# Kernel tuning notes

Hardware: AMD Instinct MI355X
Metric: run time of the kernel (lower is better)

The kernel has to match this reference:

```python
import jax, jax.numpy as jnp
import numpy as np

B, N, M, D, H, DFF = 1, 2048, 2048, 1024, 16, 4096
MASK_VAL = -50000.0
EPS = 1e-5


def _xavier(k, shape):
    lim = np.sqrt(6.0 / (shape[0] + shape[1])).astype(np.float32)
    return jax.random.uniform(k, shape, jnp.float32, -lim, lim)


def setup_inputs() -> dict:
    key = jax.random.key(0)
    ks = jax.random.split(key, 8)
    return {
        "x": jax.random.normal(ks[0], (B, N, D), jnp.float32),
        "context": jax.random.normal(ks[1], (B, M, D), jnp.float32),
        "Wq": _xavier(ks[2], (D, D)), "bq": jnp.zeros((D,), jnp.float32),
        "Wkv": _xavier(ks[3], (D, 2 * D)), "bkv": jnp.zeros((2 * D,), jnp.float32),
        "Wo": _xavier(ks[4], (D, D)), "bo": jnp.zeros((D,), jnp.float32),
        "ln1_g": jnp.ones((D,), jnp.float32), "ln1_b": jnp.zeros((D,), jnp.float32),
        "W1": _xavier(ks[5], (D, DFF)), "bf1": jnp.zeros((DFF,), jnp.float32),
        "W2": _xavier(ks[6], (DFF, D)), "bf2": jnp.zeros((D,), jnp.float32),
        "ln2_g": jnp.ones((D,), jnp.float32), "ln2_b": jnp.zeros((D,), jnp.float32),
    }


def _layernorm(x, g, b):
    mu = x.mean(-1, keepdims=True)
    var = ((x - mu) ** 2).mean(-1, keepdims=True)
    return (x - mu) * jax.lax.rsqrt(var + EPS) * g + b


def reference(x, context, Wq, bq, Wkv, bkv, Wo, bo, ln1_g, ln1_b, W1, bf1, W2, bf2, ln2_g, ln2_b):
    b, n, d = x.shape
    m = context.shape[1]
    h = H
    dh = d // h
    scale = dh ** -0.5
    # q from x only; k,v from [x; context]
    q = (x @ Wq + bq).reshape(b, n, h, dh).transpose(0, 2, 1, 3)          # b h n dh
    kv_in = jnp.concatenate([x, context], axis=1)                          # b (n+m) d
    k, v = jnp.split(kv_in @ Wkv + bkv, 2, axis=-1)
    k = k.reshape(b, n + m, h, dh).transpose(0, 2, 1, 3)                   # b h (n+m) dh
    v = v.reshape(b, n + m, h, dh).transpose(0, 2, 1, 3)
    dots = jnp.einsum('bhid,bhjd->bhij', q * scale, k)                     # b h n (n+m)
    # causal mask applies only to the self-attention (first n) key columns
    rows = jnp.arange(n)[:, None]
    cols = jnp.arange(n + m)[None, :]
    causal = (cols < n) & (cols > rows)
    dots = jnp.where(causal, MASK_VAL, dots)
    attn = jax.nn.softmax(dots, axis=-1)                                   # dropout = identity (eval)
    out = jnp.einsum('bhij,bhjd->bhid', attn, v)
    out = out.transpose(0, 2, 1, 3).reshape(b, n, d) @ Wo + bo
    # PostNorm(Residual(attn))
    x1 = _layernorm(x + out, ln1_g, ln1_b)
    # PostNorm(Residual(FFN)) with exact-erf GELU
    ff = jax.nn.gelu(x1 @ W1 + bf1, approximate=False) @ W2 + bf2
    return _layernorm(x1 + ff, ln2_g, ln2_b)
```

## Files before the change

### kernel.cpp

```cpp
#include <hip/hip_runtime.h>


using bf16x8 = __attribute__((ext_vector_type(8))) short;
using f32x4  = __attribute__((ext_vector_type(4))) float;

__device__ __forceinline__ ushort f2bf(float f) {
    unsigned u = __float_as_uint(f);
    unsigned r = (u + 0x7fffu + ((u >> 16) & 1u)) >> 16;
    return (ushort)r;
}

__device__ __forceinline__ void gload16(const void* g, void* l) {
    __builtin_amdgcn_global_load_lds(
        (const __attribute__((address_space(1))) void*)g,
        (__attribute__((address_space(3))) void*)l, 16, 0, 0);
}

__device__ __forceinline__ float gelu_erf(float v) {
    return 0.5f * v * (1.0f + erff(v * 0.70710678118654752f));
}

__device__ __forceinline__ uint cvtpk(float a, float b) {
    uint r;
    asm("v_cvt_pk_bf16_f32 %0, %1, %2" : "=v"(r) : "v"(a), "v"(b));
    return r;
}

__global__ __launch_bounds__(256) void cvt4(const float* __restrict__ in,
                                            ushort* __restrict__ out, int n) {
    int i = (blockIdx.x * 256 + threadIdx.x) * 4;
    if (i + 3 < n) {
        float4 v = *(const float4*)(in + i);
        ushort4 o;
        o.x = f2bf(v.x); o.y = f2bf(v.y); o.z = f2bf(v.z); o.w = f2bf(v.w);
        *(ushort4*)(out + i) = o;
    }
}

__global__ __launch_bounds__(256) void tcvt(const float* __restrict__ in,
                                            ushort* __restrict__ out, int R, int C) {
    __shared__ float tile[32][33];
    const int tx = threadIdx.x, ty = threadIdx.y;
    const int c0 = blockIdx.x * 32, r0 = blockIdx.y * 32;
#pragma unroll
    for (int i = 0; i < 4; ++i)
        tile[ty + 8 * i][tx] = in[(size_t)(r0 + ty + 8 * i) * C + c0 + tx];
    __syncthreads();
#pragma unroll
    for (int i = 0; i < 4; ++i)
        out[(size_t)(c0 + ty + 8 * i) * R + r0 + tx] = f2bf(tile[tx][ty + 8 * i]);
}

__global__ __launch_bounds__(256) void vtrans(const ushort* __restrict__ KV,
                                              ushort* __restrict__ Vt) {
    __shared__ ushort tile[32][34];
    const int tx = threadIdx.x, ty = threadIdx.y;
    const int j0 = blockIdx.x * 32, d0 = blockIdx.y * 32;
#pragma unroll
    for (int i = 0; i < 4; ++i)
        tile[ty + 8 * i][tx] = KV[(size_t)(j0 + ty + 8 * i) * 2048 + 1024 + d0 + tx];
    __syncthreads();
#pragma unroll
    for (int i = 0; i < 4; ++i)
        Vt[(size_t)(d0 + ty + 8 * i) * 4096 + j0 + tx] = tile[tx][ty + 8 * i];
}

template <int BM, int BN, int ACT, int OUTF32, int RES, int SCALED, int SPLITK>
__global__ __launch_bounds__(256) void gemm_bt(
    const ushort* __restrict__ A, int lda, const ushort* __restrict__ Bt, int ldb,
    const float* __restrict__ bias, const float* __restrict__ resid,
    void* __restrict__ Cout, int M, int N, int K, float scale) {
    constexpr int MR = BM / 32, NR = BN / 32;
    __shared__ __align__(16) ushort Asm[BM * 64];
    __shared__ __align__(16) ushort Bsm[BN * 64];
    const int tid = threadIdx.x;
    const int w = tid >> 6, lane = tid & 63, g = lane >> 4, i15 = lane & 15;
    const int wm = w >> 1, wn = w & 1;
    const int m0 = blockIdx.y * BM, n0 = blockIdx.x * BN;
    if (SPLITK) {
        A += (size_t)blockIdx.z * K;
        Bt += (size_t)blockIdx.z * K;
    }

    f32x4 acc[MR][NR] = {};

    for (int kt = 0; kt < K; kt += 64) {
#pragma unroll
        for (int q = 0; q < BM / 32; ++q) {
            int off = (w * (BM / 32) + q) * 1024 + lane * 16;
            int r = off >> 7, cb = off & 127;
            int scb = cb ^ ((r & 7) << 4);
            const void* src = (const char*)A + ((size_t)(m0 + r) * lda + kt) * 2 + scb;
            gload16(src, (char*)Asm + (w * (BM / 32) + q) * 1024);
        }
#pragma unroll
        for (int q = 0; q < BN / 32; ++q) {
            int off = (w * (BN / 32) + q) * 1024 + lane * 16;
            int r = off >> 7, cb = off & 127;
            int scb = cb ^ ((r & 7) << 4);
            const void* src = (const char*)Bt + ((size_t)(n0 + r) * ldb + kt) * 2 + scb;
            gload16(src, (char*)Bsm + (w * (BN / 32) + q) * 1024);
        }
        __syncthreads();

#pragma unroll
        for (int kc = 0; kc < 2; ++kc) {
            bf16x8 af[MR], bfr[NR];
#pragma unroll
            for (int mi = 0; mi < MR; ++mi) {
                int r = wm * (BM / 2) + mi * 16 + i15;
                af[mi] = *(const bf16x8*)((const char*)Asm + r * 128 +
                                          ((kc * 64 + g * 16) ^ ((r & 7) << 4)));
            }
#pragma unroll
            for (int ni = 0; ni < NR; ++ni) {
                int r = wn * (BN / 2) + ni * 16 + i15;
                bfr[ni] = *(const bf16x8*)((const char*)Bsm + r * 128 +
                                           ((kc * 64 + g * 16) ^ ((r & 7) << 4)));
            }
#pragma unroll
            for (int mi = 0; mi < MR; ++mi)
#pragma unroll
                for (int ni = 0; ni < NR; ++ni)
                    acc[mi][ni] = __builtin_amdgcn_mfma_f32_16x16x32_bf16(
                        af[mi], bfr[ni], acc[mi][ni], 0, 0, 0);
        }
        __syncthreads();
    }

    float* Cf = (float*)Cout;
    if (SPLITK) Cf += (size_t)blockIdx.z * M * N;

#pragma unroll
    for (int ni = 0; ni < NR; ++ni) {
        int col = n0 + wn * (BN / 2) + ni * 16 + i15;
        float bb = bias ? bias[col] : 0.f;
#pragma unroll
        for (int mi = 0; mi < MR; ++mi) {
#pragma unroll
            for (int r2 = 0; r2 < 4; ++r2) {
                int row = m0 + wm * (BM / 2) + mi * 16 + 4 * g + r2;
                float v = acc[mi][ni][r2] + bb;
                if (ACT) v = gelu_erf(v);
                if (SCALED) v *= scale;
                size_t off = (size_t)row * N + col;
                if (OUTF32) {
                    float rv = RES ? resid[off] : 0.f;
                    Cf[off] = v + rv;
                } else {
                    ((ushort*)Cout)[off] = f2bf(v);
                }
            }
        }
    }
}

template <int SPLIT>
__global__ __launch_bounds__(256) void flash_attn(
    const ushort* __restrict__ Q,
    const ushort* __restrict__ KVb,
    const ushort* __restrict__ Vt,
    ushort* __restrict__ O,
    float* __restrict__ Opart,
    float* __restrict__ Ml) {
    constexpr int D = 1024;
    __shared__ __align__(16) ushort Ksm[2][64 * 64];
    __shared__ __align__(16) ushort Vsm[2][64 * 64];
    __shared__ __align__(16) ushort Psm[4][16 * 64];

    const int tid = threadIdx.x;
    const int w = tid >> 6, lane = tid & 63, g = lane >> 4, i15 = lane & 15;
    const int bid = blockIdx.x;
    const int h = bid & 15;
    int qi, s;
    if (SPLIT) { qi = 31 - ((bid >> 4) >> 1); s = (bid >> 4) & 1; }
    else       { qi = 31 - (bid >> 4); s = 0; }
    const int qb = qi * 64;
    const int qrow = qb + w * 16 + i15;

    bf16x8 qf[2];
    qf[0] = *(const bf16x8*)(Q + (size_t)qrow * D + h * 64 + g * 8);
    qf[1] = *(const bf16x8*)(Q + (size_t)qrow * D + h * 64 + 32 + g * 8);

    f32x4 o[4] = {};
    float m_run = -INFINITY, l_run = 0.f;

    const int diag = qi;
    const int nt = diag + 33;
    const int lo = (SPLIT && s) ? (nt >> 1) : 0;
    const int hi = SPLIT ? (s ? nt : (nt >> 1)) : nt;

    const int sr  = tid >> 3;
    const int scb = (tid & 7) * 16;
    const int ssw = scb ^ ((sr & 7) << 4);
    const char* kb0 = (const char*)KVb + ((size_t)sr * 2048 + h * 64) * 2 + scb;
    const char* vb0 = (const char*)Vt + ((size_t)(h * 64 + sr) * 4096) * 2 + scb;

    uint4 kreg0, kreg1, vreg0, vreg1;
    auto jt_of = [&](int t) { return (t <= diag) ? t : (32 + (t - diag - 1)); };
    auto stage = [&](int jt) {
        const char* kb = kb0 + (size_t)jt * 64 * 2048 * 2;
        kreg0 = *(const uint4*)kb;
        kreg1 = *(const uint4*)(kb + 32 * 2048 * 2);
        const char* vb = vb0 + (size_t)jt * 64 * 2;
        vreg0 = *(const uint4*)vb;
        vreg1 = *(const uint4*)(vb + 32 * 4096 * 2);
    };
    auto wlds = [&](int buf) {
        *(uint4*)((char*)Ksm[buf] + sr * 128 + ssw) = kreg0;
        *(uint4*)((char*)Ksm[buf] + (sr + 32) * 128 + ssw) = kreg1;
        *(uint4*)((char*)Vsm[buf] + sr * 128 + ssw) = vreg0;
        *(uint4*)((char*)Vsm[buf] + (sr + 32) * 128 + ssw) = vreg1;
    };

    stage(jt_of(lo));
    wlds(0);
    __syncthreads();
    int cur = 0;

    const int pbase = i15 * 128;
    const int psw = (i15 & 7) << 4;

    for (int t = lo; t < hi; ++t) {
        const int jt = jt_of(t);
        const bool more = (t + 1 < hi);
        if (more) stage(jt_of(t + 1));

        f32x4 st[4];
#pragma unroll
        for (int jg = 0; jg < 4; ++jg) {
            int jr = jg * 16 + i15;
            bf16x8 ka0 = *(const bf16x8*)((const char*)Ksm[cur] + jr * 128 +
                                          ((g * 16) ^ ((jr & 7) << 4)));
            bf16x8 ka1 = *(const bf16x8*)((const char*)Ksm[cur] + jr * 128 +
                                          ((64 + g * 16) ^ ((jr & 7) << 4)));
            f32x4 z = {};
            z = __builtin_amdgcn_mfma_f32_16x16x32_bf16(ka0, qf[0], z, 0, 0, 0);
            z = __builtin_amdgcn_mfma_f32_16x16x32_bf16(ka1, qf[1], z, 0, 0, 0);
            st[jg] = z;
        }
        if (jt == diag) {
#pragma unroll
            for (int jg = 0; jg < 4; ++jg)
#pragma unroll
                for (int r = 0; r < 4; ++r) {
                    int j = jt * 64 + jg * 16 + 4 * g + r;
                    if (j > qrow) st[jg][r] = -50000.f;
                }
        }

        float v8[8];
#pragma unroll
        for (int jg = 0; jg < 4; ++jg) {
            v8[2 * jg]     = fmaxf(st[jg][0], st[jg][1]);
            v8[2 * jg + 1] = fmaxf(st[jg][2], st[jg][3]);
        }
        v8[0] = fmaxf(v8[0], v8[4]); v8[1] = fmaxf(v8[1], v8[5]);
        v8[2] = fmaxf(v8[2], v8[6]); v8[3] = fmaxf(v8[3], v8[7]);
        float mt = fmaxf(fmaxf(v8[0], v8[1]), fmaxf(v8[2], v8[3]));
        mt = fmaxf(mt, __shfl_xor(mt, 16));
        mt = fmaxf(mt, __shfl_xor(mt, 32));

        const bool skip = __all(mt - m_run <= 8.f);
        float mnew, fscale;
        if (skip) { mnew = m_run; fscale = 1.f; }
        else      { mnew = fmaxf(m_run, mt); fscale = exp2f(m_run - mnew); }

        float pf[4][4], sj[4];
#pragma unroll
        for (int jg = 0; jg < 4; ++jg) {
#pragma unroll
            for (int r = 0; r < 4; ++r) pf[jg][r] = exp2f(st[jg][r] - mnew);
            sj[jg] = (pf[jg][0] + pf[jg][1]) + (pf[jg][2] + pf[jg][3]);
        }
        float psum = (sj[0] + sj[1]) + (sj[2] + sj[3]);
        psum += __shfl_xor(psum, 16);
        psum += __shfl_xor(psum, 32);
        l_run = l_run * fscale + psum;
        m_run = mnew;

        if (!skip) {
#pragma unroll
            for (int r = 0; r < 4; ++r) {
                float fr = __shfl(fscale, 20 * g + r);
#pragma unroll
                for (int dg = 0; dg < 4; ++dg) o[dg][r] *= fr;
            }
        }

#pragma unroll
        for (int jg = 0; jg < 4; ++jg) {
            uint2 pk;
            pk.x = cvtpk(pf[jg][0], pf[jg][1]);
            pk.y = cvtpk(pf[jg][2], pf[jg][3]);
            *(uint2*)((char*)Psm[w] + pbase + ((jg * 32 + g * 8) ^ psw)) = pk;
        }

#pragma unroll
        for (int jc = 0; jc < 2; ++jc) {
            bf16x8 pa = *(const bf16x8*)((const char*)Psm[w] + pbase +
                                         ((jc * 64 + g * 16) ^ psw));
#pragma unroll
            for (int dg = 0; dg < 4; ++dg) {
                int dr = dg * 16 + i15;
                bf16x8 vb = *(const bf16x8*)((const char*)Vsm[cur] + dr * 128 +
                                             ((jc * 64 + g * 16) ^ ((dr & 7) << 4)));
                o[dg] = __builtin_amdgcn_mfma_f32_16x16x32_bf16(pa, vb, o[dg], 0, 0, 0);
            }
        }

        if (more) wlds(cur ^ 1);
        __syncthreads();
        cur ^= 1;
    }

    if (SPLIT) {
        if (g == 0) {
            float* mp = Ml + ((size_t)(s * 2048 + qb + w * 16 + i15) * 16 + h) * 2;
            mp[0] = m_run; mp[1] = l_run;
        }
#pragma unroll
        for (int r = 0; r < 4; ++r)
#pragma unroll
            for (int dg = 0; dg < 4; ++dg) {
                int row = qb + w * 16 + 4 * g + r;
                int col = h * 64 + dg * 16 + i15;
                Opart[(size_t)(s * 2048 + row) * 1024 + col] = o[dg][r];
            }
    } else {
#pragma unroll
        for (int r = 0; r < 4; ++r) {
            float lr = __shfl(l_run, 20 * g + r);
            float inv = 1.f / lr;
#pragma unroll
            for (int dg = 0; dg < 4; ++dg) {
                int row = qb + w * 16 + 4 * g + r;
                int col = h * 64 + dg * 16 + i15;
                O[(size_t)row * D + col] = f2bf(o[dg][r] * inv);
            }
        }
    }
}

__global__ __launch_bounds__(256) void attn_combine(
    const float* __restrict__ Opart, const float* __restrict__ Ml,
    ushort* __restrict__ O) {
    const int row = blockIdx.x, tid = threadIdx.x;
    const int c = tid * 4, h = c >> 6;
    const float* mp0 = Ml + ((size_t)row * 16 + h) * 2;
    const float* mp1 = Ml + ((size_t)(2048 + row) * 16 + h) * 2;
    float m0 = mp0[0], l0 = mp0[1], m1 = mp1[0], l1 = mp1[1];
    float m = fmaxf(m0, m1);
    float w0 = exp2f(m0 - m), w1 = exp2f(m1 - m);
    float inv = 1.f / (l0 * w0 + l1 * w1);
    float4 a = *(const float4*)(Opart + (size_t)row * 1024 + c);
    float4 b = *(const float4*)(Opart + (size_t)(2048 + row) * 1024 + c);
    ushort4 ob;
    ob.x = f2bf((a.x * w0 + b.x * w1) * inv);
    ob.y = f2bf((a.y * w0 + b.y * w1) * inv);
    ob.z = f2bf((a.z * w0 + b.z * w1) * inv);
    ob.w = f2bf((a.w * w0 + b.w * w1) * inv);
    *(ushort4*)(O + (size_t)row * 1024 + c) = ob;
}

__global__ __launch_bounds__(256) void layernorm_k(
    const float* __restrict__ in, const float* __restrict__ gam,
    const float* __restrict__ bet, float* __restrict__ outf,
    ushort* __restrict__ outb) {
    const int row = blockIdx.x, tid = threadIdx.x;
    const float4 v = *(const float4*)(in + (size_t)row * 1024 + tid * 4);
    float s = v.x + v.y + v.z + v.w;
    float sq = v.x * v.x + v.y * v.y + v.z * v.z + v.w * v.w;
#pragma unroll
    for (int d = 1; d < 64; d <<= 1) {
        s += __shfl_xor(s, d);
        sq += __shfl_xor(sq, d);
    }
    __shared__ float red[8];
    const int w = tid >> 6;
    if ((tid & 63) == 0) { red[w] = s; red[4 + w] = sq; }
    __syncthreads();
    s = red[0] + red[1] + red[2] + red[3];
    sq = red[4] + red[5] + red[6] + red[7];
    const float mu = s * (1.f / 1024.f);
    const float rs = rsqrtf(sq * (1.f / 1024.f) - mu * mu + 1e-5f);
    const float4 gg = *(const float4*)(gam + tid * 4);
    const float4 bb = *(const float4*)(bet + tid * 4);
    float4 o;
    o.x = (v.x - mu) * rs * gg.x + bb.x;
    o.y = (v.y - mu) * rs * gg.y + bb.y;
    o.z = (v.z - mu) * rs * gg.z + bb.z;
    o.w = (v.w - mu) * rs * gg.w + bb.w;
    *(float4*)(outf + (size_t)row * 1024 + tid * 4) = o;
    if (outb) {
        ushort4 ob;
        ob.x = f2bf(o.x); ob.y = f2bf(o.y); ob.z = f2bf(o.z); ob.w = f2bf(o.w);
        *(ushort4*)(outb + (size_t)row * 1024 + tid * 4) = ob;
    }
}

template <int NP>
__global__ __launch_bounds__(256) void layernorm_comb(
    const float* __restrict__ P,
    const float* __restrict__ bias, const float* __restrict__ resid,
    const float* __restrict__ gam, const float* __restrict__ bet,
    float* __restrict__ outf) {
    const int row = blockIdx.x, tid = threadIdx.x;
    const float4 rr = *(const float4*)(resid + (size_t)row * 1024 + tid * 4);
    const float4 bs = *(const float4*)(bias + tid * 4);
    float4 v;
    v.x = rr.x + bs.x; v.y = rr.y + bs.y; v.z = rr.z + bs.z; v.w = rr.w + bs.w;
#pragma unroll
    for (int p = 0; p < NP; ++p) {
        const float4 a = *(const float4*)(P + (size_t)(p * 2048 + row) * 1024 + tid * 4);
        v.x += a.x; v.y += a.y; v.z += a.z; v.w += a.w;
    }
    float s = v.x + v.y + v.z + v.w;
    float sq = v.x * v.x + v.y * v.y + v.z * v.z + v.w * v.w;
#pragma unroll
    for (int d = 1; d < 64; d <<= 1) {
        s += __shfl_xor(s, d);
        sq += __shfl_xor(sq, d);
    }
    __shared__ float red[8];
    const int w = tid >> 6;
    if ((tid & 63) == 0) { red[w] = s; red[4 + w] = sq; }
    __syncthreads();
    s = red[0] + red[1] + red[2] + red[3];
    sq = red[4] + red[5] + red[6] + red[7];
    const float mu = s * (1.f / 1024.f);
    const float rs = rsqrtf(sq * (1.f / 1024.f) - mu * mu + 1e-5f);
    const float4 gg = *(const float4*)(gam + tid * 4);
    const float4 bb = *(const float4*)(bet + tid * 4);
    float4 o;
    o.x = (v.x - mu) * rs * gg.x + bb.x;
    o.y = (v.y - mu) * rs * gg.y + bb.y;
    o.z = (v.z - mu) * rs * gg.z + bb.z;
    o.w = (v.w - mu) * rs * gg.w + bb.w;
    *(float4*)(outf + (size_t)row * 1024 + tid * 4) = o;
}

extern "C" void kernel_launch(void* const* d_in, const int* in_sizes, int n_in,
                              void* d_out, int out_size, void* d_ws, size_t ws_size,
                              hipStream_t stream) {
    const float* x    = (const float*)d_in[0];
    const float* ctx  = (const float*)d_in[1];
    const float* Wq   = (const float*)d_in[2];
    const float* bq   = (const float*)d_in[3];
    const float* Wkv  = (const float*)d_in[4];
    const float* bkv  = (const float*)d_in[5];
    const float* Wo   = (const float*)d_in[6];
    const float* bo   = (const float*)d_in[7];
    const float* g1   = (const float*)d_in[8];
    const float* b1   = (const float*)d_in[9];
    const float* W1   = (const float*)d_in[10];
    const float* bf1  = (const float*)d_in[11];
    const float* W2   = (const float*)d_in[12];
    const float* bf2  = (const float*)d_in[13];
    const float* g2   = (const float*)d_in[14];
    const float* b2   = (const float*)d_in[15];

    char* ws = (char*)d_ws;
    const size_t MB = 1u << 20;
    ushort* XCb  = (ushort*)(ws + 0);
    ushort* WoT  = (ushort*)(ws + 8 * MB);
    ushort* W1T  = (ushort*)(ws + 10 * MB);
    ushort* W2T  = (ushort*)(ws + 18 * MB);
    ushort* WqT  = (ushort*)(ws + 26 * MB);
    ushort* WkvT = (ushort*)(ws + 28 * MB);
    ushort* Qs   = (ushort*)(ws + 32 * MB);
    ushort* attn = (ushort*)(ws + 36 * MB);
    ushort* KV   = (ushort*)(ws + 40 * MB);
    ushort* Vt   = (ushort*)(ws + 56 * MB);
    ushort* x1b  = (ushort*)(ws + 26 * MB);
    float*  x1f  = (float*)(ws + 32 * MB);
    ushort* ffb  = (ushort*)(ws + 40 * MB);
    float*  y1   = (float*)(ws + 56 * MB);
    float*  Opart = (float*)(ws + 64 * MB);
    float*  Ml    = (float*)(ws + 80 * MB);
    float*  Pk4   = (float*)(ws + 64 * MB);
    float*  Pk2   = (float*)(ws + 0);

    cvt4<<<2048, 256, 0, stream>>>(x, XCb, 2048 * 1024);
    cvt4<<<2048, 256, 0, stream>>>(ctx, XCb + 2048 * 1024, 2048 * 1024);
    tcvt<<<dim3(32, 32), dim3(32, 8), 0, stream>>>(Wq, WqT, 1024, 1024);
    tcvt<<<dim3(64, 32), dim3(32, 8), 0, stream>>>(Wkv, WkvT, 1024, 2048);
    tcvt<<<dim3(32, 32), dim3(32, 8), 0, stream>>>(Wo, WoT, 1024, 1024);
    tcvt<<<dim3(128, 32), dim3(32, 8), 0, stream>>>(W1, W1T, 1024, 4096);
    tcvt<<<dim3(32, 128), dim3(32, 8), 0, stream>>>(W2, W2T, 4096, 1024);
    gemm_bt<64, 128, 0, 0, 0, 1, 0><<<dim3(8, 32), 256, 0, stream>>>(
        XCb, 1024, WqT, 1024, bq, nullptr, Qs, 2048, 1024, 1024, 0.18033688011112042f);
    gemm_bt<128, 128, 0, 0, 0, 0, 0><<<dim3(16, 32), 256, 0, stream>>>(
        XCb, 1024, WkvT, 1024, bkv, nullptr, KV, 4096, 2048, 1024, 1.f);
    vtrans<<<dim3(128, 32), dim3(32, 8), 0, stream>>>(KV, Vt);

    const bool split = ws_size >= 81 * MB;
    if (split) {
        flash_attn<1><<<1024, 256, 0, stream>>>(Qs, KV, Vt, nullptr, Opart, Ml);
        attn_combine<<<2048, 256, 0, stream>>>(Opart, Ml, attn);
    } else {
        flash_attn<0><<<512, 256, 0, stream>>>(Qs, KV, Vt, attn, nullptr, nullptr);
    }

    gemm_bt<64, 128, 0, 1, 1, 0, 0><<<dim3(8, 32), 256, 0, stream>>>(
        attn, 1024, WoT, 1024, bo, x, y1, 2048, 1024, 1024, 1.f);
    layernorm_k<<<2048, 256, 0, stream>>>(y1, g1, b1, x1f, x1b);
    gemm_bt<128, 128, 1, 0, 0, 0, 0><<<dim3(32, 16), 256, 0, stream>>>(
        x1b, 1024, W1T, 1024, bf1, nullptr, ffb, 2048, 4096, 1024, 1.f);
    if (ws_size >= 96 * MB) {
        gemm_bt<128, 128, 0, 1, 0, 0, 1><<<dim3(8, 16, 4), 256, 0, stream>>>(
            ffb, 4096, W2T, 4096, nullptr, nullptr, Pk4, 2048, 1024, 1024, 1.f);
        layernorm_comb<4><<<2048, 256, 0, stream>>>(Pk4, bf2, x1f, g2, b2,
                                                    (float*)d_out);
    } else {
        gemm_bt<128, 128, 0, 1, 0, 0, 1><<<dim3(8, 16, 2), 256, 0, stream>>>(
            ffb, 4096, W2T, 4096, nullptr, nullptr, Pk2, 2048, 1024, 2048, 1.f);
        layernorm_comb<2><<<2048, 256, 0, stream>>>(Pk2, bf2, x1f, g2, b2,
                                                    (float*)d_out);
    }
}
```

Before: 234.5 us.

## Use 128-row query blocks with 8 waves and 4-way KV split in flash attention

Flash attention blocks now cover 128 query rows with 512 threads (8 waves) sharing each K/V tile in LDS, which halves the K/V staging traffic per query row. The key range is split NS ways (4 when the workspace allows) to keep the grid size up, and the combine kernel is generalised to NS partials. The loop is manually unrolled over two buffers so the per-iteration buffer index disappears. In exchange there are more partial outputs to write and combine, a larger diagonal masking region per block, and more LDS and register pressure per block.

```diff
diff --git a/kernel.cpp b/kernel.cpp
--- a/kernel.cpp
+++ b/kernel.cpp
@@ -155,8 +155,8 @@
     }
 }
 
-template <int SPLIT>
-__global__ __launch_bounds__(256) void flash_attn(
+template <int NS>
+__global__ __launch_bounds__(512) void flash_attn(
     const ushort* __restrict__ Q,
     const ushort* __restrict__ KVb,
     const ushort* __restrict__ Vt,
@@ -166,17 +166,21 @@
     constexpr int D = 1024;
     __shared__ __align__(16) ushort Ksm[2][64 * 64];
     __shared__ __align__(16) ushort Vsm[2][64 * 64];
-    __shared__ __align__(16) ushort Psm[4][16 * 64];
+    __shared__ __align__(16) ushort Psm[8][16 * 64];
 
     const int tid = threadIdx.x;
     const int w = tid >> 6, lane = tid & 63, g = lane >> 4, i15 = lane & 15;
     const int bid = blockIdx.x;
     const int h = bid & 15;
-    int qi, s;
-    if (SPLIT) { qi = 31 - ((bid >> 4) >> 1); s = (bid >> 4) & 1; }
-    else       { qi = 31 - (bid >> 4); s = 0; }
-    const int qb = qi * 64;
-    const int qrow = qb + w * 16 + i15;
+    const int qB = 15 - ((bid >> 4) & 15);
+    const int s = (NS > 1) ? (bid >> 8) : 0;
+    const int qb = qB * 128 + w * 16;
+    const int qrow = qb + i15;
+    const int diagW = qb >> 6;
+    const int diagB = 2 * qB + 1;
+    const int nt = diagB + 33;
+    const int lo = (s * nt) / NS;
+    const int hi = ((s + 1) * nt) / NS;
 
     bf16x8 qf[2];
     qf[0] = *(const bf16x8*)(Q + (size_t)qrow * D + h * 64 + g * 8);
@@ -184,11 +188,6 @@
 
     f32x4 o[4] = {};
     float m_run = -INFINITY, l_run = 0.f;
-
-    const int diag = qi;
-    const int nt = diag + 33;
-    const int lo = (SPLIT && s) ? (nt >> 1) : 0;
-    const int hi = SPLIT ? (s ? nt : (nt >> 1)) : nt;
 
     const int sr  = tid >> 3;
     const int scb = (tid & 7) * 16;
@@ -196,50 +195,37 @@
     const char* kb0 = (const char*)KVb + ((size_t)sr * 2048 + h * 64) * 2 + scb;
     const char* vb0 = (const char*)Vt + ((size_t)(h * 64 + sr) * 4096) * 2 + scb;
 
-    uint4 kreg0, kreg1, vreg0, vreg1;
-    auto jt_of = [&](int t) { return (t <= diag) ? t : (32 + (t - diag - 1)); };
-    auto stage = [&](int jt) {
-        const char* kb = kb0 + (size_t)jt * 64 * 2048 * 2;
-        kreg0 = *(const uint4*)kb;
-        kreg1 = *(const uint4*)(kb + 32 * 2048 * 2);
-        const char* vb = vb0 + (size_t)jt * 64 * 2;
-        vreg0 = *(const uint4*)vb;
-        vreg1 = *(const uint4*)(vb + 32 * 4096 * 2);
+    uint4 kreg, vreg;
+    auto jt_of = [&](int t) { return (t <= diagB) ? t : (32 + (t - diagB - 1)); };
+    auto stage = [&](int t) {
+        const int jt = jt_of(t);
+        kreg = *(const uint4*)(kb0 + (size_t)jt * 64 * 4096);
+        vreg = *(const uint4*)(vb0 + (size_t)jt * 128);
     };
     auto wlds = [&](int buf) {
-        *(uint4*)((char*)Ksm[buf] + sr * 128 + ssw) = kreg0;
-        *(uint4*)((char*)Ksm[buf] + (sr + 32) * 128 + ssw) = kreg1;
-        *(uint4*)((char*)Vsm[buf] + sr * 128 + ssw) = vreg0;
-        *(uint4*)((char*)Vsm[buf] + (sr + 32) * 128 + ssw) = vreg1;
+        *(uint4*)((char*)Ksm[buf] + sr * 128 + ssw) = kreg;
+        *(uint4*)((char*)Vsm[buf] + sr * 128 + ssw) = vreg;
     };
-
-    stage(jt_of(lo));
-    wlds(0);
-    __syncthreads();
-    int cur = 0;
 
     const int pbase = i15 * 128;
     const int psw = (i15 & 7) << 4;
 
-    for (int t = lo; t < hi; ++t) {
+    auto body = [&](int buf, int t) {
         const int jt = jt_of(t);
-        const bool more = (t + 1 < hi);
-        if (more) stage(jt_of(t + 1));
-
         f32x4 st[4];
 #pragma unroll
         for (int jg = 0; jg < 4; ++jg) {
             int jr = jg * 16 + i15;
-            bf16x8 ka0 = *(const bf16x8*)((const char*)Ksm[cur] + jr * 128 +
+            bf16x8 ka0 = *(const bf16x8*)((const char*)Ksm[buf] + jr * 128 +
                                           ((g * 16) ^ ((jr & 7) << 4)));
-            bf16x8 ka1 = *(const bf16x8*)((const char*)Ksm[cur] + jr * 128 +
+            bf16x8 ka1 = *(const bf16x8*)((const char*)Ksm[buf] + jr * 128 +
                                           ((64 + g * 16) ^ ((jr & 7) << 4)));
             f32x4 z = {};
             z = __builtin_amdgcn_mfma_f32_16x16x32_bf16(ka0, qf[0], z, 0, 0, 0);
             z = __builtin_amdgcn_mfma_f32_16x16x32_bf16(ka1, qf[1], z, 0, 0, 0);
             st[jg] = z;
         }
-        if (jt == diag) {
+        if (jt >= diagW && jt <= diagB) {
 #pragma unroll
             for (int jg = 0; jg < 4; ++jg)
 #pragma unroll
@@ -303,27 +289,39 @@
 #pragma unroll
             for (int dg = 0; dg < 4; ++dg) {
                 int dr = dg * 16 + i15;
-                bf16x8 vb = *(const bf16x8*)((const char*)Vsm[cur] + dr * 128 +
+                bf16x8 vb = *(const bf16x8*)((const char*)Vsm[buf] + dr * 128 +
                                              ((jc * 64 + g * 16) ^ ((dr & 7) << 4)));
                 o[dg] = __builtin_amdgcn_mfma_f32_16x16x32_bf16(pa, vb, o[dg], 0, 0, 0);
             }
         }
-
-        if (more) wlds(cur ^ 1);
+    };
+
+    stage(lo);
+    wlds(0);
+    __syncthreads();
+
+    int t = lo;
+    for (; t + 1 < hi; t += 2) {
+        stage(t + 1);
+        body(0, t);
+        wlds(1);
         __syncthreads();
-        cur ^= 1;
-    }
-
-    if (SPLIT) {
+        if (t + 2 < hi) stage(t + 2);
+        body(1, t + 1);
+        if (t + 2 < hi) { wlds(0); __syncthreads(); }
+    }
+    if (t < hi) body(0, t);
+
+    if (NS > 1) {
         if (g == 0) {
-            float* mp = Ml + ((size_t)(s * 2048 + qb + w * 16 + i15) * 16 + h) * 2;
+            float* mp = Ml + ((size_t)(s * 2048 + qrow) * 16 + h) * 2;
             mp[0] = m_run; mp[1] = l_run;
         }
 #pragma unroll
         for (int r = 0; r < 4; ++r)
 #pragma unroll
             for (int dg = 0; dg < 4; ++dg) {
-                int row = qb + w * 16 + 4 * g + r;
+                int row = qb + 4 * g + r;
                 int col = h * 64 + dg * 16 + i15;
                 Opart[(size_t)(s * 2048 + row) * 1024 + col] = o[dg][r];
             }
@@ -334,7 +332,7 @@
             float inv = 1.f / lr;
 #pragma unroll
             for (int dg = 0; dg < 4; ++dg) {
-                int row = qb + w * 16 + 4 * g + r;
+                int row = qb + 4 * g + r;
                 int col = h * 64 + dg * 16 + i15;
                 O[(size_t)row * D + col] = f2bf(o[dg][r] * inv);
             }
@@ -342,24 +340,34 @@
     }
 }
 
+template <int NS>
 __global__ __launch_bounds__(256) void attn_combine(
     const float* __restrict__ Opart, const float* __restrict__ Ml,
     ushort* __restrict__ O) {
     const int row = blockIdx.x, tid = threadIdx.x;
     const int c = tid * 4, h = c >> 6;
-    const float* mp0 = Ml + ((size_t)row * 16 + h) * 2;
-    const float* mp1 = Ml + ((size_t)(2048 + row) * 16 + h) * 2;
-    float m0 = mp0[0], l0 = mp0[1], m1 = mp1[0], l1 = mp1[1];
-    float m = fmaxf(m0, m1);
-    float w0 = exp2f(m0 - m), w1 = exp2f(m1 - m);
-    float inv = 1.f / (l0 * w0 + l1 * w1);
-    float4 a = *(const float4*)(Opart + (size_t)row * 1024 + c);
-    float4 b = *(const float4*)(Opart + (size_t)(2048 + row) * 1024 + c);
+    float ms[NS], ls[NS];
+#pragma unroll
+    for (int s = 0; s < NS; ++s) {
+        const float* mp = Ml + ((size_t)(s * 2048 + row) * 16 + h) * 2;
+        ms[s] = mp[0]; ls[s] = mp[1];
+    }
+    float m = ms[0];
+#pragma unroll
+    for (int s = 1; s < NS; ++s) m = fmaxf(m, ms[s]);
+    float denom = 0.f, wgt[NS];
+#pragma unroll
+    for (int s = 0; s < NS; ++s) { wgt[s] = exp2f(ms[s] - m); denom += ls[s] * wgt[s]; }
+    const float inv = 1.f / denom;
+    float ax = 0, ay = 0, az = 0, aw = 0;
+#pragma unroll
+    for (int s = 0; s < NS; ++s) {
+        float4 a = *(const float4*)(Opart + (size_t)(s * 2048 + row) * 1024 + c);
+        ax += a.x * wgt[s]; ay += a.y * wgt[s]; az += a.z * wgt[s]; aw += a.w * wgt[s];
+    }
     ushort4 ob;
-    ob.x = f2bf((a.x * w0 + b.x * w1) * inv);
-    ob.y = f2bf((a.y * w0 + b.y * w1) * inv);
-    ob.z = f2bf((a.z * w0 + b.z * w1) * inv);
-    ob.w = f2bf((a.w * w0 + b.w * w1) * inv);
+    ob.x = f2bf(ax * inv); ob.y = f2bf(ay * inv);
+    ob.z = f2bf(az * inv); ob.w = f2bf(aw * inv);
     *(ushort4*)(O + (size_t)row * 1024 + c) = ob;
 }
 
@@ -477,7 +485,6 @@
     ushort* ffb  = (ushort*)(ws + 40 * MB);
     float*  y1   = (float*)(ws + 56 * MB);
     float*  Opart = (float*)(ws + 64 * MB);
-    float*  Ml    = (float*)(ws + 80 * MB);
     float*  Pk4   = (float*)(ws + 64 * MB);
     float*  Pk2   = (float*)(ws + 0);
 
@@ -494,12 +501,16 @@
         XCb, 1024, WkvT, 1024, bkv, nullptr, KV, 4096, 2048, 1024, 1.f);
     vtrans<<<dim3(128, 32), dim3(32, 8), 0, stream>>>(KV, Vt);
 
-    const bool split = ws_size >= 81 * MB;
-    if (split) {
-        flash_attn<1><<<1024, 256, 0, stream>>>(Qs, KV, Vt, nullptr, Opart, Ml);
-        attn_combine<<<2048, 256, 0, stream>>>(Opart, Ml, attn);
+    if (ws_size >= 97 * MB) {
+        float* Ml = (float*)(ws + 96 * MB);
+        flash_attn<4><<<1024, 512, 0, stream>>>(Qs, KV, Vt, nullptr, Opart, Ml);
+        attn_combine<4><<<2048, 256, 0, stream>>>(Opart, Ml, attn);
+    } else if (ws_size >= 81 * MB) {
+        float* Ml = (float*)(ws + 80 * MB);
+        flash_attn<2><<<512, 512, 0, stream>>>(Qs, KV, Vt, nullptr, Opart, Ml);
+        attn_combine<2><<<2048, 256, 0, stream>>>(Opart, Ml, attn);
     } else {
-        flash_attn<0><<<512, 256, 0, stream>>>(Qs, KV, Vt, attn, nullptr, nullptr);
+        flash_attn<1><<<256, 512, 0, stream>>>(Qs, KV, Vt, attn, nullptr, nullptr);
     }
 
     gemm_bt<64, 128, 0, 1, 1, 0, 0><<<dim3(8, 32), 256, 0, stream>>>(
```

Measured after the change: 234.1 us. No clear change (-0.2%).
